# Kernel optimization log

Hardware: AMD Instinct MI355X
Metric: run time of the kernel (lower is better)

Reference implementation:

```python
import jax, jax.numpy as jnp
import numpy as np

H = 1024  # hidden_size
I = 1024  # input_size
C = 64    # hidden_channel == out_channel
B = 1     # batch_size


def act(x):
    # CustomActivation: (|x+1| - |x-1|) / 2  == clamp(x, -1, 1)
    return (jnp.abs(x + 1.0) - jnp.abs(x - 1.0)) * 0.5


def setup_inputs() -> dict:
    key = jax.random.key(0)
    ks = jax.random.split(key, 8)
    x = jax.random.normal(ks[0], (B * C, H, I), dtype=jnp.float32)
    p_mask = jax.random.normal(ks[1], (H, I), dtype=jnp.float32)
    Wp = jnp.tril(jax.random.normal(ks[2], (H, H), dtype=jnp.float32))
    Wp = Wp.at[jnp.arange(H), jnp.arange(H)].set(1.0)
    Wp_diag = jnp.ones((H,), dtype=jnp.float32)
    Wzp = jax.random.normal(ks[3], (H, H), dtype=jnp.float32)
    lim = 1.0 / np.sqrt(I)
    p_lin_w = jax.random.uniform(ks[4], (I, I), minval=-lim, maxval=lim, dtype=jnp.float32)
    p_lin_b = jnp.zeros((I,), dtype=jnp.float32)
    z_lin_w = jax.random.uniform(ks[5], (I, I), minval=-lim, maxval=lim, dtype=jnp.float32)
    z_lin_b = jnp.zeros((I,), dtype=jnp.float32)
    return {"x": x, "p_mask": p_mask, "Wp": Wp, "Wp_diag": Wp_diag, "Wzp": Wzp,
            "p_lin_w": p_lin_w, "p_lin_b": p_lin_b, "z_lin_w": z_lin_w, "z_lin_b": z_lin_b}


def reference(x, p_mask, Wp, Wp_diag, Wzp, p_lin_w, p_lin_b, z_lin_w, z_lin_b):
    # x: (C, H, I) since batch_size == 1
    # in-place no_grad processing of Wp: tril + clamp diagonal to [0,1]
    Wp_proc = jnp.tril(Wp)
    diag = jnp.clip(jnp.diagonal(Wp_proc), 0.0, 1.0)
    Wp_proc = Wp_proc.at[jnp.arange(H), jnp.arange(H)].set(diag)
    # torch mutates .data under no_grad, so grad w.r.t. Wp is identity through this step
    Wp_eff = Wp + jax.lax.stop_gradient(Wp_proc - Wp) + jnp.diag(Wp_diag)

    p_set = x * act(p_mask)  # (C, H, I), mask broadcast over channels

    # per-channel Wp @ p_set[i], batched over channels
    t = jnp.einsum('hk,cki->chi', Wp_eff, p_set)
    # p_output_layer: act -> Linear(I, I) -> act   (Linear acts on last dim)
    p_out = act(jnp.einsum('chi,ji->chj', act(t), p_lin_w) + p_lin_b)

    z = jnp.einsum('hk,cki->chi', Wzp, p_out)
    z_out = act(jnp.einsum('chi,ji->chj', act(z), z_lin_w) + z_lin_b)

    out = (p_out + z_out).reshape(B, C, H, I)  # out_channel == hidden_channel
    return out
```

## Files before the change

kernel.cpp:

```cpp
#include <hip/hip_runtime.h>
#include <hip/hip_bf16.h>


typedef short bf16x8 __attribute__((ext_vector_type(8)));
typedef float f32x4  __attribute__((ext_vector_type(4)));

__device__ __forceinline__ float actf(float v) { return fminf(1.f, fmaxf(-1.f, v)); }

__device__ __forceinline__ unsigned short f2bf(float f) {
    union { __hip_bfloat16 b; unsigned short u; } cv;
    cv.b = __float2bfloat16(f);
    return cv.u;
}
__device__ __forceinline__ float bf2f(unsigned short u) {
    union { unsigned short u; __hip_bfloat16 b; } cv;
    cv.u = u;
    return __bfloat162float(cv.b);
}

__device__ __forceinline__ int swz(int r) { return (r ^ (r >> 2)) & 3; }

__device__ __forceinline__ bf16x8 read_frag(const unsigned short* ldsBase, int row, int q) {
    const int pc = q ^ swz(row);
    return *(const bf16x8*)(ldsBase + row * 32 + pc * 8);
}

template <bool SPLIT, int EPI, bool TRIL>
__global__ __launch_bounds__(512, 2)
void gemm_tn8(const unsigned short* __restrict__ Ahi,
              const unsigned short* __restrict__ Alo,
              const unsigned short* __restrict__ Bhi,
              const unsigned short* __restrict__ Blo,
              const float* __restrict__ bias,
              const unsigned short* __restrict__ Phi,
              const unsigned short* __restrict__ Plo,
              unsigned short* __restrict__ O1,
              unsigned short* __restrict__ O2,
              float* __restrict__ Of) {
    constexpr int NOPS   = SPLIT ? 4 : 2;
    constexpr int ROUNDS = SPLIT ? 8 : 4;
    __shared__ __align__(16) unsigned short lds[NOPS * 2 * 8192];

    const int tid  = threadIdx.x;
    const int lane = tid & 63;
    const int wave = tid >> 6;
    const int wm = wave >> 2;
    const int wn = wave & 3;
    const int q  = lane >> 4;
    const int mr = lane & 15;

    const int m0 = blockIdx.y * 256;
    const int n0 = blockIdx.x * 256;
    const size_t cb = (size_t)blockIdx.z << 20;

    const unsigned short* Bh = Bhi + cb;
    const unsigned short* Bl = SPLIT ? (Blo + cb) : nullptr;

    auto stage1 = [&](const unsigned short* g, int row0, int k0,
                      unsigned short* base, int rnd) {
        const int ci = rnd * 512 + tid;
        const int r  = ci >> 2;
        const int pc = ci & 3;
        const int qq = pc ^ swz(r);
        const unsigned short* gsrc = g + ((size_t)(row0 + r) << 10) + k0 + qq * 8;
        unsigned short* ldst = base + (rnd * 512 + wave * 64) * 8;
        __builtin_amdgcn_global_load_lds((const __attribute__((address_space(1))) void*)gsrc,
                                         (__attribute__((address_space(3))) void*)ldst,
                                         16, 0, 0);
    };
    auto issueRound = [&](int idx, int k0, int buf) {
        int op, rnd;
        if constexpr (SPLIT) { op = (idx & 1) + ((idx >= 4) ? 2 : 0); rnd = (idx >> 1) & 1; }
        else                 { op = idx & 1; rnd = idx >> 1; }
        const unsigned short* g; int row0;
        switch (op) {
            case 0:  g = Ahi; row0 = m0; break;
            case 1:  g = Bh;  row0 = n0; break;
            case 2:  g = Alo; row0 = m0; break;
            default: g = Bl;  row0 = n0; break;
        }
        stage1(g, row0, k0, lds + (op * 2 + buf) * 8192, rnd);
    };

    f32x4 acc[8][4];
#pragma unroll
    for (int i = 0; i < 8; ++i)
#pragma unroll
        for (int j = 0; j < 4; ++j) acc[i][j] = (f32x4){0.f, 0.f, 0.f, 0.f};

    const int kEnd = TRIL ? ((m0 + 256 < 1024) ? m0 + 256 : 1024) : 1024;
    const int nt = kEnd >> 5;

#pragma unroll
    for (int idx = 0; idx < ROUNDS; ++idx) issueRound(idx, 0, 0);

    for (int t = 0; t < nt; ++t) {
        const int cur = t & 1;
        const int nxt = cur ^ 1;
        const int k0n = (t + 1) << 5;
        const bool pf = (t + 1) < nt;

        const unsigned short* Ah_ = lds + (0 * 2 + cur) * 8192;
        const unsigned short* Bh_ = lds + (1 * 2 + cur) * 8192;
        const unsigned short* Al_ = SPLIT ? (lds + (2 * 2 + cur) * 8192) : nullptr;
        const unsigned short* Bl_ = SPLIT ? (lds + (3 * 2 + cur) * 8192) : nullptr;

        if (pf) {
            issueRound(0, k0n, nxt);
            issueRound(1, k0n, nxt);
            asm volatile("s_waitcnt vmcnt(2)" ::: "memory");
        } else {
            asm volatile("s_waitcnt vmcnt(0)" ::: "memory");
        }
        asm volatile("s_barrier" ::: "memory");

        bf16x8 bh01[2], bl01[2], bh23[2], bl23[2];

        {
            bf16x8 aH[4], aL[4];
#pragma unroll
            for (int i = 0; i < 4; ++i) {
                aH[i] = read_frag(Ah_, wm * 128 + i * 16 + mr, q);
                if constexpr (SPLIT) aL[i] = read_frag(Al_, wm * 128 + i * 16 + mr, q);
            }
#pragma unroll
            for (int j = 0; j < 2; ++j) {
                bh01[j] = read_frag(Bh_, wn * 64 + j * 16 + mr, q);
                if constexpr (SPLIT) bl01[j] = read_frag(Bl_, wn * 64 + j * 16 + mr, q);
            }
            if (pf) { issueRound(2, k0n, nxt); issueRound(3, k0n, nxt); }
            asm volatile("s_barrier" ::: "memory");
            __builtin_amdgcn_s_setprio(1);
#pragma unroll
            for (int i = 0; i < 4; ++i)
#pragma unroll
                for (int j = 0; j < 2; ++j) {
                    if constexpr (SPLIT) {
                        acc[i][j] = __builtin_amdgcn_mfma_f32_16x16x32_bf16(aL[i], bh01[j], acc[i][j], 0, 0, 0);
                        acc[i][j] = __builtin_amdgcn_mfma_f32_16x16x32_bf16(aH[i], bl01[j], acc[i][j], 0, 0, 0);
                    }
                    acc[i][j] = __builtin_amdgcn_mfma_f32_16x16x32_bf16(aH[i], bh01[j], acc[i][j], 0, 0, 0);
                }
            __builtin_amdgcn_s_setprio(0);
            __builtin_amdgcn_sched_barrier(0);
            asm volatile("s_barrier" ::: "memory");
        }

        {
            bf16x8 aH[4], aL[4];
#pragma unroll
            for (int i = 0; i < 4; ++i) {
                aH[i] = read_frag(Ah_, wm * 128 + 64 + i * 16 + mr, q);
                if constexpr (SPLIT) aL[i] = read_frag(Al_, wm * 128 + 64 + i * 16 + mr, q);
            }
            if constexpr (SPLIT) {
                if (pf) { issueRound(4, k0n, nxt); issueRound(5, k0n, nxt); }
            }
            asm volatile("s_barrier" ::: "memory");
            __builtin_amdgcn_s_setprio(1);
#pragma unroll
            for (int i = 0; i < 4; ++i)
#pragma unroll
                for (int j = 0; j < 2; ++j) {
                    if constexpr (SPLIT) {
                        acc[i + 4][j] = __builtin_amdgcn_mfma_f32_16x16x32_bf16(aL[i], bh01[j], acc[i + 4][j], 0, 0, 0);
                        acc[i + 4][j] = __builtin_amdgcn_mfma_f32_16x16x32_bf16(aH[i], bl01[j], acc[i + 4][j], 0, 0, 0);
                    }
                    acc[i + 4][j] = __builtin_amdgcn_mfma_f32_16x16x32_bf16(aH[i], bh01[j], acc[i + 4][j], 0, 0, 0);
                }
            __builtin_amdgcn_s_setprio(0);
            __builtin_amdgcn_sched_barrier(0);
            asm volatile("s_barrier" ::: "memory");
        }

        {
            bf16x8 aH[4], aL[4];
#pragma unroll
            for (int i = 0; i < 4; ++i) {
                aH[i] = read_frag(Ah_, wm * 128 + i * 16 + mr, q);
                if constexpr (SPLIT) aL[i] = read_frag(Al_, wm * 128 + i * 16 + mr, q);
            }
#pragma unroll
            for (int j = 0; j < 2; ++j) {
                bh23[j] = read_frag(Bh_, wn * 64 + (j + 2) * 16 + mr, q);
                if constexpr (SPLIT) bl23[j] = read_frag(Bl_, wn * 64 + (j + 2) * 16 + mr, q);
            }
            if constexpr (SPLIT) {
                if (pf) { issueRound(6, k0n, nxt); issueRound(7, k0n, nxt); }
            }
            asm volatile("s_barrier" ::: "memory");
            __builtin_amdgcn_s_setprio(1);
#pragma unroll
            for (int i = 0; i < 4; ++i)
#pragma unroll
                for (int j = 0; j < 2; ++j) {
                    if constexpr (SPLIT) {
                        acc[i][j + 2] = __builtin_amdgcn_mfma_f32_16x16x32_bf16(aL[i], bh23[j], acc[i][j + 2], 0, 0, 0);
                        acc[i][j + 2] = __builtin_amdgcn_mfma_f32_16x16x32_bf16(aH[i], bl23[j], acc[i][j + 2], 0, 0, 0);
                    }
                    acc[i][j + 2] = __builtin_amdgcn_mfma_f32_16x16x32_bf16(aH[i], bh23[j], acc[i][j + 2], 0, 0, 0);
                }
            __builtin_amdgcn_s_setprio(0);
            __builtin_amdgcn_sched_barrier(0);
            asm volatile("s_barrier" ::: "memory");
        }

        {
            bf16x8 aH[4], aL[4];
#pragma unroll
            for (int i = 0; i < 4; ++i) {
                aH[i] = read_frag(Ah_, wm * 128 + 64 + i * 16 + mr, q);
                if constexpr (SPLIT) aL[i] = read_frag(Al_, wm * 128 + 64 + i * 16 + mr, q);
            }
            asm volatile("s_barrier" ::: "memory");
            __builtin_amdgcn_s_setprio(1);
#pragma unroll
            for (int i = 0; i < 4; ++i)
#pragma unroll
                for (int j = 0; j < 2; ++j) {
                    if constexpr (SPLIT) {
                        acc[i + 4][j + 2] = __builtin_amdgcn_mfma_f32_16x16x32_bf16(aL[i], bh23[j], acc[i + 4][j + 2], 0, 0, 0);
                        acc[i + 4][j + 2] = __builtin_amdgcn_mfma_f32_16x16x32_bf16(aH[i], bl23[j], acc[i + 4][j + 2], 0, 0, 0);
                    }
                    acc[i + 4][j + 2] = __builtin_amdgcn_mfma_f32_16x16x32_bf16(aH[i], bh23[j], acc[i + 4][j + 2], 0, 0, 0);
                }
            __builtin_amdgcn_s_setprio(0);
            __builtin_amdgcn_sched_barrier(0);
            asm volatile("s_barrier" ::: "memory");
        }
    }

#pragma unroll
    for (int i = 0; i < 8; ++i) {
        const int gmBase = m0 + wm * 128 + i * 16 + q * 4;
#pragma unroll
        for (int j = 0; j < 4; ++j) {
            const int gn = n0 + wn * 64 + j * 16 + mr;
#pragma unroll
            for (int r4 = 0; r4 < 4; ++r4) {
                const int gm = gmBase + r4;
                const size_t off = cb + ((size_t)gm << 10) + gn;
                float v = acc[i][j][r4];
                if constexpr (EPI == 0) {
                    O1[off] = f2bf(actf(v));
                } else if constexpr (EPI == 1) {
                    v = actf(v + bias[gm]);
                    const unsigned short hi = f2bf(v);
                    O1[off] = hi;
                    O2[off] = f2bf(v - bf2f(hi));
                } else {
                    v = actf(v + bias[gm]);
                    v += bf2f(Phi[off]) + bf2f(Plo[off]);
                    Of[off] = v;
                }
            }
        }
    }
}

__global__ void prep_weights(const float* __restrict__ Wp, const float* __restrict__ Wpd,
                             const float* __restrict__ Wzp,
                             const float* __restrict__ plw, const float* __restrict__ zlw,
                             unsigned short* __restrict__ WpHi, unsigned short* __restrict__ WpLo,
                             unsigned short* __restrict__ WzHi, unsigned short* __restrict__ WzLo,
                             unsigned short* __restrict__ plw16, unsigned short* __restrict__ zlw16) {
    const int idx = blockIdx.x * 256 + threadIdx.x;
    const int h = idx >> 10, k = idx & 1023;
    float v = (k < h) ? Wp[idx] : 0.f;
    if (k == h) v = fminf(1.f, fmaxf(0.f, Wp[idx])) + Wpd[h];
    unsigned short hi = f2bf(v);
    WpHi[idx] = hi; WpLo[idx] = f2bf(v - bf2f(hi));
    const float wz = Wzp[idx];
    hi = f2bf(wz);
    WzHi[idx] = hi; WzLo[idx] = f2bf(wz - bf2f(hi));
    plw16[idx] = f2bf(plw[idx]);
    zlw16[idx] = f2bf(zlw[idx]);
}

__global__ void prep_pset(const float* __restrict__ x, const float* __restrict__ pmask,
                          unsigned short* __restrict__ Thi, unsigned short* __restrict__ Tlo) {
    __shared__ float tile[32][33];
    const int tx = threadIdx.x, ty = threadIdx.y;
    const int i0 = blockIdx.x * 32, h0 = blockIdx.y * 32;
    const size_t cb = (size_t)blockIdx.z << 20;
#pragma unroll
    for (int s = 0; s < 4; ++s) {
        const int hh = ty + s * 8;
        const size_t gi = ((size_t)(h0 + hh) << 10) + i0 + tx;
        tile[hh][tx] = x[cb + gi] * actf(pmask[gi]);
    }
    __syncthreads();
#pragma unroll
    for (int s = 0; s < 4; ++s) {
        const int ii = ty + s * 8;
        const float v = tile[tx][ii];
        const size_t go = cb + ((size_t)(i0 + ii) << 10) + h0 + tx;
        const unsigned short hi = f2bf(v);
        Thi[go] = hi;
        Tlo[go] = f2bf(v - bf2f(hi));
    }
}

__global__ void transpose_out(const float* __restrict__ inT,
                              float* __restrict__ out) {
    __shared__ float tile[32][33];
    const int tx = threadIdx.x, ty = threadIdx.y;
    const int h0 = blockIdx.x * 32, j0 = blockIdx.y * 32;
    const size_t cb = (size_t)blockIdx.z << 20;
#pragma unroll
    for (int s = 0; s < 4; ++s) {
        const int jj = ty + s * 8;
        tile[jj][tx] = inT[cb + ((size_t)(j0 + jj) << 10) + h0 + tx];
    }
    __syncthreads();
#pragma unroll
    for (int s = 0; s < 4; ++s) {
        const int hh = ty + s * 8;
        out[cb + ((size_t)(h0 + hh) << 10) + j0 + tx] = tile[tx][hh];
    }
}

extern "C" void kernel_launch(void* const* d_in, const int* in_sizes, int n_in,
                              void* d_out, int out_size, void* d_ws, size_t ws_size,
                              hipStream_t stream) {
    const float* x     = (const float*)d_in[0];
    const float* pmask = (const float*)d_in[1];
    const float* Wp    = (const float*)d_in[2];
    const float* Wpd   = (const float*)d_in[3];
    const float* Wzp   = (const float*)d_in[4];
    const float* plw   = (const float*)d_in[5];
    const float* plb   = (const float*)d_in[6];
    const float* zlw   = (const float*)d_in[7];
    const float* zlb   = (const float*)d_in[8];
    float* out = (float*)d_out;

    char* w = (char*)d_ws;
    const size_t SZ = 134217728ull;
    unsigned short* pSetT_hi = (unsigned short*)(w);
    unsigned short* pSetT_lo = (unsigned short*)(w + SZ);
    unsigned short* pT_hi    = (unsigned short*)(w + 2 * SZ);
    unsigned short* pT_lo    = (unsigned short*)(w + 3 * SZ);
    unsigned short* tA       = (unsigned short*)(w + 4 * SZ);
    float*          outT     = (float*)(w);
    unsigned short* wts      = (unsigned short*)(w + 5 * SZ);
    unsigned short* WpHi = wts;
    unsigned short* WpLo = wts + 1 * 1048576;
    unsigned short* WzHi = wts + 2 * 1048576;
    unsigned short* WzLo = wts + 3 * 1048576;
    unsigned short* plw16 = wts + 4 * 1048576;
    unsigned short* zlw16 = wts + 5 * 1048576;

    const dim3 gW(4096), bW(256);
    const dim3 gT(32, 32, 64), bT(32, 8);
    const dim3 gG(4, 4, 64), bG(512);

    prep_weights<<<gW, bW, 0, stream>>>(Wp, Wpd, Wzp, plw, zlw,
                                        WpHi, WpLo, WzHi, WzLo, plw16, zlw16);
    prep_pset<<<gT, bT, 0, stream>>>(x, pmask, pSetT_hi, pSetT_lo);

    gemm_tn8<true, 0, true><<<gG, bG, 0, stream>>>(
        WpHi, WpLo, pSetT_hi, pSetT_lo, nullptr, nullptr, nullptr, tA, nullptr, nullptr);

    gemm_tn8<false, 1, false><<<gG, bG, 0, stream>>>(
        plw16, nullptr, tA, nullptr, plb, nullptr, nullptr, pT_hi, pT_lo, nullptr);

    gemm_tn8<true, 0, false><<<gG, bG, 0, stream>>>(
        WzHi, WzLo, pT_hi, pT_lo, nullptr, nullptr, nullptr, tA, nullptr, nullptr);

    gemm_tn8<false, 2, false><<<gG, bG, 0, stream>>>(
        zlw16, nullptr, tA, nullptr, zlb, pT_hi, pT_lo, nullptr, nullptr, outT);

    transpose_out<<<gT, bT, 0, stream>>>(outT, out);
}
```

Measured before the change: 1.783 ms.

## Fuse output transpose into final GEMM epilogue and restructure fragment reuse

The final GEMM epilogue now stages results in LDS and writes the transposed output straight to the destination tensor. This removes the separate transpose_out kernel and its extra full read and write of the fp32 output. The K-loop is also reorganized from four quarter phases into three, keeping the B fragments live so the second half of A reuses them. That cuts LDS fragment re-reads but raises register pressure. The epilogue adds barriers and LDS traffic per row group.

```diff
diff --git a/kernel.cpp b/kernel.cpp
--- a/kernel.cpp
+++ b/kernel.cpp
@@ -114,146 +114,136 @@
         }
         asm volatile("s_barrier" ::: "memory");
 
-        bf16x8 bh01[2], bl01[2], bh23[2], bl23[2];
-
-        {
-            bf16x8 aH[4], aL[4];
-#pragma unroll
-            for (int i = 0; i < 4; ++i) {
-                aH[i] = read_frag(Ah_, wm * 128 + i * 16 + mr, q);
-                if constexpr (SPLIT) aL[i] = read_frag(Al_, wm * 128 + i * 16 + mr, q);
-            }
+        bf16x8 aH[4], aL[4], bH[4], bL[4];
+#pragma unroll
+        for (int i = 0; i < 4; ++i) {
+            aH[i] = read_frag(Ah_, wm * 128 + i * 16 + mr, q);
+            if constexpr (SPLIT) aL[i] = read_frag(Al_, wm * 128 + i * 16 + mr, q);
+        }
+#pragma unroll
+        for (int j = 0; j < 2; ++j) {
+            bH[j] = read_frag(Bh_, wn * 64 + j * 16 + mr, q);
+            if constexpr (SPLIT) bL[j] = read_frag(Bl_, wn * 64 + j * 16 + mr, q);
+        }
+        if (pf) {
+            issueRound(2, k0n, nxt);
+            issueRound(3, k0n, nxt);
+            if constexpr (SPLIT) { issueRound(4, k0n, nxt); issueRound(5, k0n, nxt); }
+        }
+        asm volatile("s_barrier" ::: "memory");
+        __builtin_amdgcn_s_setprio(1);
+#pragma unroll
+        for (int i = 0; i < 4; ++i)
 #pragma unroll
             for (int j = 0; j < 2; ++j) {
-                bh01[j] = read_frag(Bh_, wn * 64 + j * 16 + mr, q);
-                if constexpr (SPLIT) bl01[j] = read_frag(Bl_, wn * 64 + j * 16 + mr, q);
-            }
-            if (pf) { issueRound(2, k0n, nxt); issueRound(3, k0n, nxt); }
+                if constexpr (SPLIT) {
+                    acc[i][j] = __builtin_amdgcn_mfma_f32_16x16x32_bf16(aL[i], bH[j], acc[i][j], 0, 0, 0);
+                    acc[i][j] = __builtin_amdgcn_mfma_f32_16x16x32_bf16(aH[i], bL[j], acc[i][j], 0, 0, 0);
+                }
+                acc[i][j] = __builtin_amdgcn_mfma_f32_16x16x32_bf16(aH[i], bH[j], acc[i][j], 0, 0, 0);
+            }
+        __builtin_amdgcn_s_setprio(0);
+        __builtin_amdgcn_sched_barrier(0);
+        asm volatile("s_barrier" ::: "memory");
+
+#pragma unroll
+        for (int j = 0; j < 2; ++j) {
+            bH[2 + j] = read_frag(Bh_, wn * 64 + (2 + j) * 16 + mr, q);
+            if constexpr (SPLIT) bL[2 + j] = read_frag(Bl_, wn * 64 + (2 + j) * 16 + mr, q);
+        }
+        if constexpr (SPLIT) {
+            if (pf) { issueRound(6, k0n, nxt); issueRound(7, k0n, nxt); }
+        }
+        asm volatile("s_barrier" ::: "memory");
+        __builtin_amdgcn_s_setprio(1);
+#pragma unroll
+        for (int i = 0; i < 4; ++i)
+#pragma unroll
+            for (int j = 0; j < 2; ++j) {
+                if constexpr (SPLIT) {
+                    acc[i][j + 2] = __builtin_amdgcn_mfma_f32_16x16x32_bf16(aL[i], bH[2 + j], acc[i][j + 2], 0, 0, 0);
+                    acc[i][j + 2] = __builtin_amdgcn_mfma_f32_16x16x32_bf16(aH[i], bL[2 + j], acc[i][j + 2], 0, 0, 0);
+                }
+                acc[i][j + 2] = __builtin_amdgcn_mfma_f32_16x16x32_bf16(aH[i], bH[2 + j], acc[i][j + 2], 0, 0, 0);
+            }
+        __builtin_amdgcn_s_setprio(0);
+        __builtin_amdgcn_sched_barrier(0);
+        asm volatile("s_barrier" ::: "memory");
+
+        bf16x8 cH[4], cL[4];
+#pragma unroll
+        for (int i = 0; i < 4; ++i) {
+            cH[i] = read_frag(Ah_, wm * 128 + 64 + i * 16 + mr, q);
+            if constexpr (SPLIT) cL[i] = read_frag(Al_, wm * 128 + 64 + i * 16 + mr, q);
+        }
+        asm volatile("s_barrier" ::: "memory");
+        __builtin_amdgcn_s_setprio(1);
+#pragma unroll
+        for (int i = 0; i < 4; ++i)
+#pragma unroll
+            for (int j = 0; j < 4; ++j) {
+                if constexpr (SPLIT) {
+                    acc[i + 4][j] = __builtin_amdgcn_mfma_f32_16x16x32_bf16(cL[i], bH[j], acc[i + 4][j], 0, 0, 0);
+                    acc[i + 4][j] = __builtin_amdgcn_mfma_f32_16x16x32_bf16(cH[i], bL[j], acc[i + 4][j], 0, 0, 0);
+                }
+                acc[i + 4][j] = __builtin_amdgcn_mfma_f32_16x16x32_bf16(cH[i], bH[j], acc[i + 4][j], 0, 0, 0);
+            }
+        __builtin_amdgcn_s_setprio(0);
+        __builtin_amdgcn_sched_barrier(0);
+        asm volatile("s_barrier" ::: "memory");
+    }
+
+    if constexpr (EPI != 2) {
+#pragma unroll
+        for (int i = 0; i < 8; ++i) {
+            const int gmBase = m0 + wm * 128 + i * 16 + q * 4;
+#pragma unroll
+            for (int j = 0; j < 4; ++j) {
+                const int gn = n0 + wn * 64 + j * 16 + mr;
+#pragma unroll
+                for (int r4 = 0; r4 < 4; ++r4) {
+                    const int gm = gmBase + r4;
+                    const size_t off = cb + ((size_t)gm << 10) + gn;
+                    float v = acc[i][j][r4];
+                    if constexpr (EPI == 0) {
+                        O1[off] = f2bf(actf(v));
+                    } else {
+                        v = actf(v + bias[gm]);
+                        const unsigned short hi = f2bf(v);
+                        O1[off] = hi;
+                        O2[off] = f2bf(v - bf2f(hi));
+                    }
+                }
+            }
+        }
+    } else {
+        float* ldsT = (float*)lds;
+#pragma unroll
+        for (int i = 0; i < 8; ++i) {
+            const int gmBase = m0 + wm * 128 + i * 16 + q * 4;
+#pragma unroll
+            for (int j = 0; j < 4; ++j) {
+                const int gn = n0 + wn * 64 + j * 16 + mr;
+#pragma unroll
+                for (int r4 = 0; r4 < 4; ++r4) {
+                    const int gm = gmBase + r4;
+                    const size_t off = cb + ((size_t)gm << 10) + gn;
+                    float v = actf(acc[i][j][r4] + bias[gm]);
+                    v += bf2f(Phi[off]) + bf2f(Plo[off]);
+                    ldsT[(wm * 16 + q * 4 + r4) * 258 + wn * 64 + j * 16 + mr] = v;
+                }
+            }
             asm volatile("s_barrier" ::: "memory");
-            __builtin_amdgcn_s_setprio(1);
-#pragma unroll
-            for (int i = 0; i < 4; ++i)
-#pragma unroll
-                for (int j = 0; j < 2; ++j) {
-                    if constexpr (SPLIT) {
-                        acc[i][j] = __builtin_amdgcn_mfma_f32_16x16x32_bf16(aL[i], bh01[j], acc[i][j], 0, 0, 0);
-                        acc[i][j] = __builtin_amdgcn_mfma_f32_16x16x32_bf16(aH[i], bl01[j], acc[i][j], 0, 0, 0);
-                    }
-                    acc[i][j] = __builtin_amdgcn_mfma_f32_16x16x32_bf16(aH[i], bh01[j], acc[i][j], 0, 0, 0);
-                }
-            __builtin_amdgcn_s_setprio(0);
-            __builtin_amdgcn_sched_barrier(0);
-            asm volatile("s_barrier" ::: "memory");
-        }
-
-        {
-            bf16x8 aH[4], aL[4];
-#pragma unroll
-            for (int i = 0; i < 4; ++i) {
-                aH[i] = read_frag(Ah_, wm * 128 + 64 + i * 16 + mr, q);
-                if constexpr (SPLIT) aL[i] = read_frag(Al_, wm * 128 + 64 + i * 16 + mr, q);
-            }
-            if constexpr (SPLIT) {
-                if (pf) { issueRound(4, k0n, nxt); issueRound(5, k0n, nxt); }
-            }
-            asm volatile("s_barrier" ::: "memory");
-            __builtin_amdgcn_s_setprio(1);
-#pragma unroll
-            for (int i = 0; i < 4; ++i)
-#pragma unroll
-                for (int j = 0; j < 2; ++j) {
-                    if constexpr (SPLIT) {
-                        acc[i + 4][j] = __builtin_amdgcn_mfma_f32_16x16x32_bf16(aL[i], bh01[j], acc[i + 4][j], 0, 0, 0);
-                        acc[i + 4][j] = __builtin_amdgcn_mfma_f32_16x16x32_bf16(aH[i], bl01[j], acc[i + 4][j], 0, 0, 0);
-                    }
-                    acc[i + 4][j] = __builtin_amdgcn_mfma_f32_16x16x32_bf16(aH[i], bh01[j], acc[i + 4][j], 0, 0, 0);
-                }
-            __builtin_amdgcn_s_setprio(0);
-            __builtin_amdgcn_sched_barrier(0);
-            asm volatile("s_barrier" ::: "memory");
-        }
-
-        {
-            bf16x8 aH[4], aL[4];
-#pragma unroll
-            for (int i = 0; i < 4; ++i) {
-                aH[i] = read_frag(Ah_, wm * 128 + i * 16 + mr, q);
-                if constexpr (SPLIT) aL[i] = read_frag(Al_, wm * 128 + i * 16 + mr, q);
-            }
-#pragma unroll
-            for (int j = 0; j < 2; ++j) {
-                bh23[j] = read_frag(Bh_, wn * 64 + (j + 2) * 16 + mr, q);
-                if constexpr (SPLIT) bl23[j] = read_frag(Bl_, wn * 64 + (j + 2) * 16 + mr, q);
-            }
-            if constexpr (SPLIT) {
-                if (pf) { issueRound(6, k0n, nxt); issueRound(7, k0n, nxt); }
-            }
-            asm volatile("s_barrier" ::: "memory");
-            __builtin_amdgcn_s_setprio(1);
-#pragma unroll
-            for (int i = 0; i < 4; ++i)
-#pragma unroll
-                for (int j = 0; j < 2; ++j) {
-                    if constexpr (SPLIT) {
-                        acc[i][j + 2] = __builtin_amdgcn_mfma_f32_16x16x32_bf16(aL[i], bh23[j], acc[i][j + 2], 0, 0, 0);
-                        acc[i][j + 2] = __builtin_amdgcn_mfma_f32_16x16x32_bf16(aH[i], bl23[j], acc[i][j + 2], 0, 0, 0);
-                    }
-                    acc[i][j + 2] = __builtin_amdgcn_mfma_f32_16x16x32_bf16(aH[i], bh23[j], acc[i][j + 2], 0, 0, 0);
-                }
-            __builtin_amdgcn_s_setprio(0);
-            __builtin_amdgcn_sched_barrier(0);
-            asm volatile("s_barrier" ::: "memory");
-        }
-
-        {
-            bf16x8 aH[4], aL[4];
-#pragma unroll
-            for (int i = 0; i < 4; ++i) {
-                aH[i] = read_frag(Ah_, wm * 128 + 64 + i * 16 + mr, q);
-                if constexpr (SPLIT) aL[i] = read_frag(Al_, wm * 128 + 64 + i * 16 + mr, q);
-            }
-            asm volatile("s_barrier" ::: "memory");
-            __builtin_amdgcn_s_setprio(1);
-#pragma unroll
-            for (int i = 0; i < 4; ++i)
-#pragma unroll
-                for (int j = 0; j < 2; ++j) {
-                    if constexpr (SPLIT) {
-                        acc[i + 4][j + 2] = __builtin_amdgcn_mfma_f32_16x16x32_bf16(aL[i], bh23[j], acc[i + 4][j + 2], 0, 0, 0);
-                        acc[i + 4][j + 2] = __builtin_amdgcn_mfma_f32_16x16x32_bf16(aH[i], bl23[j], acc[i + 4][j + 2], 0, 0, 0);
-                    }
-                    acc[i + 4][j + 2] = __builtin_amdgcn_mfma_f32_16x16x32_bf16(aH[i], bh23[j], acc[i + 4][j + 2], 0, 0, 0);
-                }
-            __builtin_amdgcn_s_setprio(0);
-            __builtin_amdgcn_sched_barrier(0);
-            asm volatile("s_barrier" ::: "memory");
-        }
-    }
-
-#pragma unroll
-    for (int i = 0; i < 8; ++i) {
-        const int gmBase = m0 + wm * 128 + i * 16 + q * 4;
-#pragma unroll
-        for (int j = 0; j < 4; ++j) {
-            const int gn = n0 + wn * 64 + j * 16 + mr;
-#pragma unroll
-            for (int r4 = 0; r4 < 4; ++r4) {
-                const int gm = gmBase + r4;
-                const size_t off = cb + ((size_t)gm << 10) + gn;
-                float v = acc[i][j][r4];
-                if constexpr (EPI == 0) {
-                    O1[off] = f2bf(actf(v));
-                } else if constexpr (EPI == 1) {
-                    v = actf(v + bias[gm]);
-                    const unsigned short hi = f2bf(v);
-                    O1[off] = hi;
-                    O2[off] = f2bf(v - bf2f(hi));
-                } else {
-                    v = actf(v + bias[gm]);
-                    v += bf2f(Phi[off]) + bf2f(Plo[off]);
-                    Of[off] = v;
-                }
-            }
+#pragma unroll
+            for (int s = 0; s < 16; ++s) {
+                const int idx = s * 512 + tid;
+                const int hh  = idx >> 5;
+                const int jl  = idx & 31;
+                const int jg  = m0 + (jl >> 4) * 128 + i * 16 + (jl & 15);
+                const int hg  = n0 + hh;
+                Of[cb + ((size_t)hg << 10) + jg] = ldsT[jl * 258 + hh];
+            }
+            if (i != 7) asm volatile("s_barrier" ::: "memory");
         }
     }
 }
@@ -301,25 +291,6 @@
     }
 }
 
-__global__ void transpose_out(const float* __restrict__ inT,
-                              float* __restrict__ out) {
-    __shared__ float tile[32][33];
-    const int tx = threadIdx.x, ty = threadIdx.y;
-    const int h0 = blockIdx.x * 32, j0 = blockIdx.y * 32;
-    const size_t cb = (size_t)blockIdx.z << 20;
-#pragma unroll
-    for (int s = 0; s < 4; ++s) {
-        const int jj = ty + s * 8;
-        tile[jj][tx] = inT[cb + ((size_t)(j0 + jj) << 10) + h0 + tx];
-    }
-    __syncthreads();
-#pragma unroll
-    for (int s = 0; s < 4; ++s) {
-        const int hh = ty + s * 8;
-        out[cb + ((size_t)(h0 + hh) << 10) + j0 + tx] = tile[tx][hh];
-    }
-}
-
 extern "C" void kernel_launch(void* const* d_in, const int* in_sizes, int n_in,
                               void* d_out, int out_size, void* d_ws, size_t ws_size,
                               hipStream_t stream) {
@@ -341,7 +312,6 @@
     unsigned short* pT_hi    = (unsigned short*)(w + 2 * SZ);
     unsigned short* pT_lo    = (unsigned short*)(w + 3 * SZ);
     unsigned short* tA       = (unsigned short*)(w + 4 * SZ);
-    float*          outT     = (float*)(w);
     unsigned short* wts      = (unsigned short*)(w + 5 * SZ);
     unsigned short* WpHi = wts;
     unsigned short* WpLo = wts + 1 * 1048576;
@@ -368,7 +338,5 @@
         WzHi, WzLo, pT_hi, pT_lo, nullptr, nullptr, nullptr, tA, nullptr, nullptr);
 
     gemm_tn8<false, 2, false><<<gG, bG, 0, stream>>>(
-        zlw16, nullptr, tA, nullptr, zlb, pT_hi, pT_lo, nullptr, nullptr, outT);
-
-    transpose_out<<<gT, bT, 0, stream>>>(outT, out);
-}
+        zlw16, nullptr, tA, nullptr, zlb, pT_hi, pT_lo, nullptr, nullptr, out);
+}
```

Measured after the change: 1.597 ms. 1.12x faster.
